# Kernel optimization log

Hardware: AMD Instinct MI355X
Metric: run time of the kernel (lower is better)

Reference implementation:

```python
import jax, jax.numpy as jnp
from jax import lax
import numpy as np

# Graph / tensor dims
N = 64          # regular nodes (each has a ResistiveTensor state)
N1 = N + 1      # + virtual input node (original node -1), zero state, source-only
E = 513         # 512 random edges + 1 input edge; each edge has its own Reverb conv
B, C, H, W = 8, 3, 64, 64
K = 4           # Reverb kernel_size
EQ = -0.1       # ResistiveTensor equilibrium


def setup_inputs() -> dict:
    key = jax.random.key(0)
    ks = jax.random.split(key, 7)
    states = jax.random.normal(ks[0], (N1, B, C, H, W), jnp.float32)
    states = states.at[N].set(0.0)  # virtual input node has zero state
    noise = jax.random.normal(ks[1], (N1, B, C, H, W), jnp.float32) * 0.05
    conv_w = jax.random.normal(ks[2], (E, C, C, K, K), jnp.float32) * 0.1
    conv_b = jax.random.normal(ks[3], (E, C), jnp.float32) * 0.01
    resistivity = jax.random.uniform(ks[4], (N, B, C, H, W), jnp.float32)
    src = jax.random.randint(ks[5], (E,), 0, N1)   # sources may include input node N
    dst = jax.random.randint(ks[6], (E,), 0, N)    # targets are regular nodes only
    return dict(states=states, noise=noise, conv_w=conv_w, conv_b=conv_b,
                resistivity=resistivity, src=src, dst=dst)


def _conv_same(x, w, b):
    # x: [B,C,H,W], w: [Cout,Cin,K,K]; even kernel -> asymmetric SAME padding (1,2)
    y = lax.conv_general_dilated(x, w, (1, 1), [(1, 2), (1, 2)],
                                 dimension_numbers=('NCHW', 'OIHW', 'NCHW'))
    return y + b[None, :, None, None]


def reference(states, noise, conv_w, conv_b, resistivity, src, dst):
    # Phase 1: per-node activation (with injected noise), as in time_step
    acts = jax.nn.sigmoid(states + noise)            # [N1,B,C,H,W]
    # Phase 2: per-edge gather -> Reverb conv -> scatter-add into target states
    edge_in = acts[src]                              # [E,B,C,H,W] gather
    updates = jax.vmap(_conv_same)(edge_in, conv_w, conv_b)  # [E,B,C,H,W]
    agg = jax.ops.segment_sum(updates, dst, num_segments=N1)  # scatter-add by target
    # ResistiveTensor accumulate: pull toward equilibrium scaled by |resistivity|
    new_states = states + agg
    new_states = new_states.at[:N].add(jnp.abs(resistivity) * (EQ - states[:N]))
    return new_states
```

## Files before the change

### kernel.cpp

```cpp
#include <hip/hip_runtime.h>

#define NN 64
#define BB 8
#define HH 64
#define WW 64
#define EE 513
#define EQF -0.1f
#define IMG 4096
#define CHW 12288

typedef unsigned short u16;
typedef __attribute__((ext_vector_type(8))) short bf16x8;
typedef __attribute__((ext_vector_type(4))) float f32x4;

#define ROWS_P 67
#define B_STR (ROWS_P * 256)
#define N_STR (BB * B_STR)

#define TROW_B 528
#define TILE_B (11 * TROW_B)
#define NPIECE 352

__device__ __forceinline__ u16 f2bf(float f) {
  union { float f; unsigned u; } c; c.f = f;
  return (u16)((c.u + 0x7fffu + ((c.u >> 16) & 1u)) >> 16);
}

__device__ __forceinline__ void wg_barrier() {
  asm volatile("s_waitcnt lgkmcnt(0)\n\ts_barrier" ::: "memory");
  __builtin_amdgcn_sched_barrier(0);
}

__global__ __launch_bounds__(512) void pre_k(const float* __restrict__ conv_w,
                                             const float* __restrict__ conv_b,
                                             const int* __restrict__ src,
                                             const int* __restrict__ dst,
                                             const float* __restrict__ states,
                                             const float* __restrict__ noise,
                                             const float* __restrict__ res,
                                             u16* __restrict__ actsI,
                                             u16* __restrict__ wfrag,
                                             int* __restrict__ csr_off,
                                             int2* __restrict__ csr2,
                                             float* __restrict__ nodeBias,
                                             int* __restrict__ nodePerm,
                                             float* __restrict__ out) {
  __shared__ int sdst[EE];
  __shared__ int ssrc[EE];
  __shared__ int swcnt[8][64];
  __shared__ int spw[8][64];
  __shared__ int soffs[NN + 1];
  __shared__ int slist[EE];
  const int tid = threadIdx.x;
  const int bid = blockIdx.x;

  if (bid == 0) {
    for (int e = tid; e < EE; e += 512) { sdst[e] = dst[e]; ssrc[e] = src[e]; }
    __syncthreads();
    const int wv = tid >> 6, l = tid & 63;
    const int d = sdst[tid];
    int rank = 0, cnt = 0;
    for (int i = 0; i < 64; ++i) {
      int di = __shfl(d, i, 64);
      rank += (di == d && i < l) ? 1 : 0;
      cnt  += (di == l) ? 1 : 0;
    }
    swcnt[wv][l] = cnt;
    __syncthreads();
    if (tid < 64) {
      int s = 0;
      #pragma unroll
      for (int w2 = 0; w2 < 8; ++w2) { spw[w2][tid] = s; s += swcnt[w2][tid]; }
      int tot = s + ((sdst[512] == tid) ? 1 : 0);
      int scan = tot;
      #pragma unroll
      for (int ofs = 1; ofs < 64; ofs <<= 1) {
        int v = __shfl_up(scan, ofs, 64);
        if (tid >= ofs) scan += v;
      }
      soffs[tid] = scan - tot;
      if (tid == 63) soffs[64] = scan;
      int prank = 0;
      #pragma unroll
      for (int m = 0; m < 64; ++m) {
        int cm = __shfl(tot, m, 64);
        prank += (cm > tot || (cm == tot && m < tid)) ? 1 : 0;
      }
      nodePerm[prank] = tid;
    }
    __syncthreads();
    slist[soffs[d] + spw[wv][d] + rank] = tid;
    if (tid == 0) { int d5 = sdst[512]; slist[soffs[d5 + 1] - 1] = 512; }
    __syncthreads();
    if (tid <= NN) csr_off[tid] = soffs[tid];
    for (int q = tid; q < EE; q += 512) {
      int ee = slist[q];
      csr2[q] = make_int2(ssrc[ee] * N_STR, ee * 512);
    }
    if (tid < 192) {
      int n = tid / 3, co = tid - n * 3;
      float s = 0.f;
      for (int q = soffs[n]; q < soffs[n + 1]; ++q)
        s += conv_b[slist[q] * 3 + co];
      nodeBias[tid] = s;
    }
  } else if (bid <= 65) {
    int gid = (bid - 1) * 512 + tid;
    if (gid < EE * 64) {
      int e = gid >> 6, l = gid & 63;
      int g = l >> 4, col = l & 15, co = col >> 2, kw = col & 3;
      u16 v[8];
      #pragma unroll
      for (int j = 0; j < 8; ++j) {
        float f = 0.0f;
        if (co < 3 && j < 3) f = conv_w[e * 144 + co * 48 + j * 16 + g * 4 + kw];
        v[j] = f2bf(f);
      }
      uint4 pk;
      pk.x = (unsigned)v[0] | ((unsigned)v[1] << 16);
      pk.y = (unsigned)v[2] | ((unsigned)v[3] << 16);
      pk.z = (unsigned)v[4] | ((unsigned)v[5] << 16);
      pk.w = (unsigned)v[6] | ((unsigned)v[7] << 16);
      *(uint4*)(wfrag + (size_t)gid * 8) = pk;
    }
  } else {
    int idx = (bid - 66) * 512 + tid;
    int w4 = idx & 15, h = (idx >> 4) & 63, b = (idx >> 10) & 7, n = idx >> 13;
    int pbase = (n * 8 + b) * CHW + h * 64 + w4 * 4;
    float4 s0 = *(const float4*)(states + pbase);
    float4 s1 = *(const float4*)(states + pbase + IMG);
    float4 s2 = *(const float4*)(states + pbase + 2 * IMG);
    float4 z0 = *(const float4*)(noise + pbase);
    float4 z1 = *(const float4*)(noise + pbase + IMG);
    float4 z2 = *(const float4*)(noise + pbase + 2 * IMG);
    float a0[4], a1[4], a2[4];
    #pragma unroll
    for (int p = 0; p < 4; ++p) {
      float v0 = ((const float*)&s0)[p] + ((const float*)&z0)[p];
      float v1 = ((const float*)&s1)[p] + ((const float*)&z1)[p];
      float v2 = ((const float*)&s2)[p] + ((const float*)&z2)[p];
      a0[p] = 1.0f / (1.0f + __expf(-v0));
      a1[p] = 1.0f / (1.0f + __expf(-v1));
      a2[p] = 1.0f / (1.0f + __expf(-v2));
    }
    uint4 q0, q1;
    q0.x = (unsigned)f2bf(a0[0]) | ((unsigned)f2bf(a1[0]) << 16);
    q0.y = (unsigned)f2bf(a2[0]);
    q0.z = (unsigned)f2bf(a0[1]) | ((unsigned)f2bf(a1[1]) << 16);
    q0.w = (unsigned)f2bf(a2[1]);
    q1.x = (unsigned)f2bf(a0[2]) | ((unsigned)f2bf(a1[2]) << 16);
    q1.y = (unsigned)f2bf(a2[2]);
    q1.z = (unsigned)f2bf(a0[3]) | ((unsigned)f2bf(a1[3]) << 16);
    q1.w = (unsigned)f2bf(a2[3]);
    u16* dp = actsI + (size_t)((n * 8 + b) * ROWS_P + (h + 1)) * 256 + w4 * 16;
    *(uint4*)dp = q0;
    *(uint4*)(dp + 8) = q1;
    uint4 zz; zz.x = 0u; zz.y = 0u; zz.z = 0u; zz.w = 0u;
    if (h == 0) {
      u16* zp = actsI + (size_t)((n * 8 + b) * ROWS_P + 0) * 256 + w4 * 16;
      *(uint4*)zp = zz; *(uint4*)(zp + 8) = zz;
    }
    if (h == 63) {
      u16* zp = actsI + (size_t)((n * 8 + b) * ROWS_P + 65) * 256 + w4 * 16;
      *(uint4*)zp = zz; *(uint4*)(zp + 8) = zz;
      zp += 256;
      *(uint4*)zp = zz; *(uint4*)(zp + 8) = zz;
    }
    if (n == NN) {
      *(float4*)(out + pbase) = s0;
      *(float4*)(out + pbase + IMG) = s1;
      *(float4*)(out + pbase + 2 * IMG) = s2;
    } else {
      float4 r0 = *(const float4*)(res + pbase);
      float4 r1 = *(const float4*)(res + pbase + IMG);
      float4 r2 = *(const float4*)(res + pbase + 2 * IMG);
      float4 o0, o1, o2;
      #pragma unroll
      for (int p = 0; p < 4; ++p) {
        ((float*)&o0)[p] = ((const float*)&s0)[p] + fabsf(((const float*)&r0)[p]) * (EQF - ((const float*)&s0)[p]);
        ((float*)&o1)[p] = ((const float*)&s1)[p] + fabsf(((const float*)&r1)[p]) * (EQF - ((const float*)&s1)[p]);
        ((float*)&o2)[p] = ((const float*)&s2)[p] + fabsf(((const float*)&r2)[p]) * (EQF - ((const float*)&s2)[p]);
      }
      *(float4*)(out + pbase) = o0;
      *(float4*)(out + pbase + IMG) = o1;
      *(float4*)(out + pbase + 2 * IMG) = o2;
    }
  }
}

__global__ __launch_bounds__(256, 5) void conv_k(const u16* __restrict__ actsI,
                                                 const u16* __restrict__ wfrag,
                                                 const int* __restrict__ csr_off,
                                                 const int2* __restrict__ csr2,
                                                 const float* __restrict__ nodeBias,
                                                 const int* __restrict__ nodePerm,
                                                 float* __restrict__ out) {
  __shared__ __align__(16) char smem[13312];

  const int tid = threadIdx.x, lane = tid & 63, wid = tid >> 6;
  const int bid = blockIdx.x;
  const int n = nodePerm[bid >> 6];
  const int b = (bid >> 3) & 7, ht = bid & 7;
  const int R0 = ht * 8;

  int pg[2], pl[2];
  #pragma unroll
  for (int j = 0; j < 2; ++j) {
    int p = tid + j * 256;
    int row = p >> 5, c16 = p & 31;
    pg[j] = b * B_STR + (R0 + row) * 256 + c16 * 8;
    pl[j] = row * TROW_B + c16 * 16;
  }
  const bool pv1 = tid < (NPIECE - 256);

  const int g = lane >> 4, px = lane & 15;
  const int abase = (wid * 2 + g) * TROW_B + px * 8;

  f32x4 acc[2][4];
  #pragma unroll
  for (int h2 = 0; h2 < 2; ++h2)
    #pragma unroll
    for (int t = 0; t < 4; ++t) { acc[h2][t][0]=0.f; acc[h2][t][1]=0.f; acc[h2][t][2]=0.f; acc[h2][t][3]=0.f; }

  const int e0 = csr_off[n], cnt = csr_off[n + 1] - e0;

  uint4 a0, a1; bf16x8 wa;
  uint4 b0, b1; bf16x8 wb;

#define LOADP(R0_,R1_,WF_,I_) do {                                            \
    int2 c_ = csr2[e0 + (I_)];                                                \
    int sx_ = __builtin_amdgcn_readfirstlane(c_.x);                           \
    int wx_ = __builtin_amdgcn_readfirstlane(c_.y);                           \
    const u16* ap_ = actsI + sx_;                                             \
    R0_ = *(const uint4*)(ap_ + pg[0]);                                       \
    if (pv1) R1_ = *(const uint4*)(ap_ + pg[1]);                              \
    WF_ = *(const bf16x8*)(wfrag + wx_ + lane * 8);                           \
  } while (0)

#define STOREP(R0_,R1_,BOFS_) do {                                            \
    *(uint4*)(smem + (BOFS_) + pl[0]) = R0_;                                  \
    if (pv1) *(uint4*)(smem + (BOFS_) + pl[1]) = R1_;                         \
  } while (0)

#define COMP(BOFS_,WF_) do {                                                  \
    _Pragma("unroll")                                                         \
    for (int h2_ = 0; h2_ < 2; ++h2_) {                                       \
      _Pragma("unroll")                                                       \
      for (int t_ = 0; t_ < 4; ++t_) {                                        \
        short4 d_ = *(const short4*)(smem + (BOFS_) + abase + h2_ * TROW_B + t_ * 128); \
        bf16x8 av_;                                                           \
        av_[0]=d_.x; av_[1]=d_.y; av_[2]=d_.z; av_[3]=d_.w;                   \
        av_[4]=0; av_[5]=0; av_[6]=0; av_[7]=0;                               \
        acc[h2_][t_] = __builtin_amdgcn_mfma_f32_16x16x32_bf16(av_, WF_, acc[h2_][t_], 0, 0, 0); \
      }                                                                       \
    }                                                                         \
  } while (0)

#define PHASE(R0_,R1_,WF_,NEXTI_) do {                                        \
    STOREP(R0_, R1_, bofs);                                                   \
    bf16x8 wcur_ = WF_;                                                       \
    if ((NEXTI_) < cnt) LOADP(R0_, R1_, WF_, (NEXTI_));                       \
    wg_barrier();                                                             \
    COMP(bofs, wcur_);                                                        \
    bofs ^= TILE_B;                                                           \
  } while (0)

  if (cnt > 0) LOADP(a0, a1, wa, 0);
  if (cnt > 1) LOADP(b0, b1, wb, 1);
  int bofs = 0;
  int i = 0;
  for (; i + 1 < cnt; i += 2) {
    PHASE(a0, a1, wa, i + 2);
    PHASE(b0, b1, wb, i + 3);
  }
  if (i < cnt) PHASE(a0, a1, wa, cnt);

  __syncthreads();
  float* zr = (float*)(smem + wid * 3328);
  const float bc0 = nodeBias[n * 3 + 0];
  const float bc1 = nodeBias[n * 3 + 1];
  const float bc2 = nodeBias[n * 3 + 2];
  const int col = lane & 15;
  #pragma unroll
  for (int h2 = 0; h2 < 2; ++h2) {
    if (col < 12) {
      #pragma unroll
      for (int t = 0; t < 4; ++t)
        #pragma unroll
        for (int r = 0; r < 4; ++r)
          zr[(t * 16 + g * 4 + r) * 13 + col] = acc[h2][t][r];
    }
    int hr = R0 + wid * 2 + h2;
    #pragma unroll
    for (int co = 0; co < 3; ++co) {
      float y = (co == 0) ? bc0 : ((co == 1) ? bc1 : bc2);
      #pragma unroll
      for (int kw = 0; kw < 4; ++kw) {
        int wp = lane + kw - 1;
        if (wp >= 0 && wp < 64) y += zr[wp * 13 + co * 4 + kw];
      }
      int o = ((n * 8 + b) * 3 + co) * IMG + hr * 64 + lane;
      out[o] += y;
    }
  }
}

extern "C" void kernel_launch(void* const* d_in, const int* in_sizes, int n_in,
                              void* d_out, int out_size, void* d_ws, size_t ws_size,
                              hipStream_t stream) {
  const float* states = (const float*)d_in[0];
  const float* noise  = (const float*)d_in[1];
  const float* conv_w = (const float*)d_in[2];
  const float* conv_b = (const float*)d_in[3];
  const float* res    = (const float*)d_in[4];
  const int*   src    = (const int*)d_in[5];
  const int*   dst    = (const int*)d_in[6];
  float* out = (float*)d_out;

  u16* actsI = (u16*)d_ws;
  u16* wfrag = (u16*)((char*)d_ws + 17838080);
  int* csr_off = (int*)((char*)d_ws + 18363392);
  int2* csr2 = (int2*)((char*)d_ws + 18363712);
  float* nodeBias = (float*)((char*)d_ws + 18367816);
  int* nodePerm = (int*)((char*)d_ws + 18368584);

  pre_k<<<1106, 512, 0, stream>>>(conv_w, conv_b, src, dst, states, noise, res,
                                  actsI, wfrag, csr_off, csr2, nodeBias, nodePerm, out);
  conv_k<<<4096, 256, 0, stream>>>(actsI, wfrag, csr_off, csr2, nodeBias, nodePerm, out);
}
```

Before: 55.30 us.

## Use direct global-to-LDS loads with 4-buffer pipeline and smaller row tiles

The conv kernel now loads activation tiles straight into LDS with global_load_lds, which removes the register staging and the LDS store step. It keeps a four-buffer ring with vmcnt-based waits so more edges stay in flight. Each block covers 4 output rows instead of 8, which doubles the grid to 8192 blocks and raises the occupancy hint, and the per-node edge list is cached in LDS. The trade-off is more halo reloading per output row and more blocks. The edge count per node is also capped at 72 by the LDS edge cache.

New measurement: 103.3 us. 86.8% more time.

```diff
diff --git a/kernel.cpp b/kernel.cpp
--- a/kernel.cpp
+++ b/kernel.cpp
@@ -17,19 +17,29 @@
 #define B_STR (ROWS_P * 256)
 #define N_STR (BB * B_STR)
 
-#define TROW_B 528
-#define TILE_B (11 * TROW_B)
-#define NPIECE 352
+#define TILE_B 3584
+#define B0 0
+#define B1 3584
+#define B2 7168
+#define B3 10752
+#define SCSR_OFF 14336
+#define MAXE 72
 
 __device__ __forceinline__ u16 f2bf(float f) {
   union { float f; unsigned u; } c; c.f = f;
   return (u16)((c.u + 0x7fffu + ((c.u >> 16) & 1u)) >> 16);
 }
 
-__device__ __forceinline__ void wg_barrier() {
-  asm volatile("s_waitcnt lgkmcnt(0)\n\ts_barrier" ::: "memory");
-  __builtin_amdgcn_sched_barrier(0);
-}
+__device__ __forceinline__ void gld16(const void* gsrc, void* ldst) {
+  typedef __attribute__((address_space(1))) const unsigned int gu32;
+  typedef __attribute__((address_space(3))) unsigned int lu32;
+  __builtin_amdgcn_global_load_lds((gu32*)gsrc, (lu32*)ldst, 16, 0, 0);
+}
+
+#define WAITBAR(N) do {                                                       \
+    asm volatile("s_waitcnt vmcnt(" #N ")\n\ts_barrier" ::: "memory");        \
+    __builtin_amdgcn_sched_barrier(0);                                        \
+  } while (0)
 
 __global__ __launch_bounds__(512) void pre_k(const float* __restrict__ conv_w,
                                              const float* __restrict__ conv_b,
@@ -188,92 +198,76 @@
   }
 }
 
-__global__ __launch_bounds__(256, 5) void conv_k(const u16* __restrict__ actsI,
+__global__ __launch_bounds__(256, 6) void conv_k(const u16* __restrict__ actsI,
                                                  const u16* __restrict__ wfrag,
                                                  const int* __restrict__ csr_off,
-                                                 const int2* __restrict__ csr2,
+                                                 const int2* __restrict__ csr2g,
                                                  const float* __restrict__ nodeBias,
                                                  const int* __restrict__ nodePerm,
                                                  float* __restrict__ out) {
-  __shared__ __align__(16) char smem[13312];
+  __shared__ __align__(16) char smem[SCSR_OFF + MAXE * 8];
 
   const int tid = threadIdx.x, lane = tid & 63, wid = tid >> 6;
   const int bid = blockIdx.x;
-  const int n = nodePerm[bid >> 6];
-  const int b = (bid >> 3) & 7, ht = bid & 7;
-  const int R0 = ht * 8;
-
-  int pg[2], pl[2];
+  const int n = nodePerm[bid >> 7];
+  const int b = (bid >> 4) & 7, ht = bid & 15;
+  const int R0 = ht * 4;
+
+  const int prow = tid >> 5, pc16 = tid & 31;
+  const int pg = b * B_STR + (R0 + prow) * 256 + pc16 * 8;
+  char* const ldst = smem + wid * 1024;
+
+  const int g = lane >> 4, px = lane & 15;
+  const int abase = (wid + g) * 512 + px * 8;
+
+  f32x4 acc[4];
   #pragma unroll
-  for (int j = 0; j < 2; ++j) {
-    int p = tid + j * 256;
-    int row = p >> 5, c16 = p & 31;
-    pg[j] = b * B_STR + (R0 + row) * 256 + c16 * 8;
-    pl[j] = row * TROW_B + c16 * 16;
-  }
-  const bool pv1 = tid < (NPIECE - 256);
-
-  const int g = lane >> 4, px = lane & 15;
-  const int abase = (wid * 2 + g) * TROW_B + px * 8;
-
-  f32x4 acc[2][4];
-  #pragma unroll
-  for (int h2 = 0; h2 < 2; ++h2)
-    #pragma unroll
-    for (int t = 0; t < 4; ++t) { acc[h2][t][0]=0.f; acc[h2][t][1]=0.f; acc[h2][t][2]=0.f; acc[h2][t][3]=0.f; }
+  for (int t = 0; t < 4; ++t) { acc[t][0]=0.f; acc[t][1]=0.f; acc[t][2]=0.f; acc[t][3]=0.f; }
 
   const int e0 = csr_off[n], cnt = csr_off[n + 1] - e0;
-
-  uint4 a0, a1; bf16x8 wa;
-  uint4 b0, b1; bf16x8 wb;
-
-#define LOADP(R0_,R1_,WF_,I_) do {                                            \
-    int2 c_ = csr2[e0 + (I_)];                                                \
+  int2* scsr = (int2*)(smem + SCSR_OFF);
+  if (tid < cnt) scsr[tid] = csr2g[e0 + tid];
+  __syncthreads();
+
+  bf16x8 wf0, wf1, wf2, wf3;
+
+#define ISSUE(BOFS_, WF_, I_) do {                                            \
+    int2 c_ = scsr[(I_)];                                                     \
     int sx_ = __builtin_amdgcn_readfirstlane(c_.x);                           \
     int wx_ = __builtin_amdgcn_readfirstlane(c_.y);                           \
-    const u16* ap_ = actsI + sx_;                                             \
-    R0_ = *(const uint4*)(ap_ + pg[0]);                                       \
-    if (pv1) R1_ = *(const uint4*)(ap_ + pg[1]);                              \
+    if (tid < 224) gld16((const void*)(actsI + sx_ + pg), ldst + (BOFS_));    \
     WF_ = *(const bf16x8*)(wfrag + wx_ + lane * 8);                           \
   } while (0)
 
-#define STOREP(R0_,R1_,BOFS_) do {                                            \
-    *(uint4*)(smem + (BOFS_) + pl[0]) = R0_;                                  \
-    if (pv1) *(uint4*)(smem + (BOFS_) + pl[1]) = R1_;                         \
-  } while (0)
-
-#define COMP(BOFS_,WF_) do {                                                  \
+#define COMP(BOFS_, WF_) do {                                                 \
     _Pragma("unroll")                                                         \
-    for (int h2_ = 0; h2_ < 2; ++h2_) {                                       \
-      _Pragma("unroll")                                                       \
-      for (int t_ = 0; t_ < 4; ++t_) {                                        \
-        short4 d_ = *(const short4*)(smem + (BOFS_) + abase + h2_ * TROW_B + t_ * 128); \
-        bf16x8 av_;                                                           \
-        av_[0]=d_.x; av_[1]=d_.y; av_[2]=d_.z; av_[3]=d_.w;                   \
-        av_[4]=0; av_[5]=0; av_[6]=0; av_[7]=0;                               \
-        acc[h2_][t_] = __builtin_amdgcn_mfma_f32_16x16x32_bf16(av_, WF_, acc[h2_][t_], 0, 0, 0); \
-      }                                                                       \
+    for (int t_ = 0; t_ < 4; ++t_) {                                          \
+      short4 d_ = *(const short4*)(smem + (BOFS_) + abase + t_ * 128);        \
+      bf16x8 av_;                                                             \
+      av_[0]=d_.x; av_[1]=d_.y; av_[2]=d_.z; av_[3]=d_.w;                     \
+      av_[4]=0; av_[5]=0; av_[6]=0; av_[7]=0;                                 \
+      acc[t_] = __builtin_amdgcn_mfma_f32_16x16x32_bf16(av_, WF_, acc[t_], 0, 0, 0); \
     }                                                                         \
   } while (0)
 
-#define PHASE(R0_,R1_,WF_,NEXTI_) do {                                        \
-    STOREP(R0_, R1_, bofs);                                                   \
-    bf16x8 wcur_ = WF_;                                                       \
-    if ((NEXTI_) < cnt) LOADP(R0_, R1_, WF_, (NEXTI_));                       \
-    wg_barrier();                                                             \
-    COMP(bofs, wcur_);                                                        \
-    bofs ^= TILE_B;                                                           \
+#define PH(CB_, WFC_, NB_, WFN_) do {                                         \
+    if (i + 2 < cnt) { ISSUE(NB_, WFN_, i + 2); WAITBAR(4); }                 \
+    else if (i + 1 < cnt) { WAITBAR(2); }                                     \
+    else { WAITBAR(0); }                                                      \
+    COMP(CB_, WFC_);                                                          \
   } while (0)
 
-  if (cnt > 0) LOADP(a0, a1, wa, 0);
-  if (cnt > 1) LOADP(b0, b1, wb, 1);
-  int bofs = 0;
-  int i = 0;
-  for (; i + 1 < cnt; i += 2) {
-    PHASE(a0, a1, wa, i + 2);
-    PHASE(b0, b1, wb, i + 3);
+  if (cnt > 0) {
+    ISSUE(B0, wf0, 0);
+    if (cnt > 1) ISSUE(B1, wf1, 1);
+    int i = 0;
+    while (true) {
+      PH(B0, wf0, B2, wf2); if (++i == cnt) break;
+      PH(B1, wf1, B3, wf3); if (++i == cnt) break;
+      PH(B2, wf2, B0, wf0); if (++i == cnt) break;
+      PH(B3, wf3, B1, wf1); if (++i == cnt) break;
+    }
   }
-  if (i < cnt) PHASE(a0, a1, wa, cnt);
 
   __syncthreads();
   float* zr = (float*)(smem + wid * 3328);
@@ -281,27 +275,24 @@
   const float bc1 = nodeBias[n * 3 + 1];
   const float bc2 = nodeBias[n * 3 + 2];
   const int col = lane & 15;
+  if (col < 12) {
+    #pragma unroll
+    for (int t = 0; t < 4; ++t)
+      #pragma unroll
+      for (int r = 0; r < 4; ++r)
+        zr[(t * 16 + g * 4 + r) * 13 + col] = acc[t][r];
+  }
+  const int hr = R0 + wid;
   #pragma unroll
-  for (int h2 = 0; h2 < 2; ++h2) {
-    if (col < 12) {
-      #pragma unroll
-      for (int t = 0; t < 4; ++t)
-        #pragma unroll
-        for (int r = 0; r < 4; ++r)
-          zr[(t * 16 + g * 4 + r) * 13 + col] = acc[h2][t][r];
-    }
-    int hr = R0 + wid * 2 + h2;
+  for (int co = 0; co < 3; ++co) {
+    float y = (co == 0) ? bc0 : ((co == 1) ? bc1 : bc2);
     #pragma unroll
-    for (int co = 0; co < 3; ++co) {
-      float y = (co == 0) ? bc0 : ((co == 1) ? bc1 : bc2);
-      #pragma unroll
-      for (int kw = 0; kw < 4; ++kw) {
-        int wp = lane + kw - 1;
-        if (wp >= 0 && wp < 64) y += zr[wp * 13 + co * 4 + kw];
-      }
-      int o = ((n * 8 + b) * 3 + co) * IMG + hr * 64 + lane;
-      out[o] += y;
-    }
+    for (int kw = 0; kw < 4; ++kw) {
+      int wp = lane + kw - 1;
+      if (wp >= 0 && wp < 64) y += zr[wp * 13 + co * 4 + kw];
+    }
+    int o = ((n * 8 + b) * 3 + co) * IMG + hr * 64 + lane;
+    out[o] += y;
   }
 }
 
@@ -326,5 +317,5 @@
 
   pre_k<<<1106, 512, 0, stream>>>(conv_w, conv_b, src, dst, states, noise, res,
                                   actsI, wfrag, csr_off, csr2, nodeBias, nodePerm, out);
-  conv_k<<<4096, 256, 0, stream>>>(actsI, wfrag, csr_off, csr2, nodeBias, nodePerm, out);
-}
+  conv_k<<<8192, 256, 0, stream>>>(actsI, wfrag, csr_off, csr2, nodeBias, nodePerm, out);
+}
```
